# Performance work log

Hardware: AMD Instinct MI355X
Metric: run time of the kernel (lower is better)

The kernel has to match this reference:

```python
import jax, jax.numpy as jnp
import numpy as np

HIDDEN = 128
CHUNK = 3
EPS = 1e-5  # BatchNorm1d eps


def conv1d(x, w, b, pad):
    # x: (B, C_in, S), w: (C_out, C_in, K)
    y = jax.lax.conv_general_dilated(x, w, window_strides=(1,), padding=[(pad, pad)],
                                     dimension_numbers=('NCH', 'OIH', 'NCH'))
    return y + b[None, :, None]


def setup_inputs() -> dict:
    key = jax.random.key(0)
    ks = jax.random.split(key, 16)
    B, S = 64, 2048
    sc = 0.05
    inp = {}
    inp['x'] = jax.random.normal(ks[0], (B, S), jnp.float32)
    inp['seq_lens'] = jax.random.randint(ks[1], (B,), 0, S).astype(jnp.int64)
    # conv stack params (layer 0 has in_channels=1)
    inp['conv_w0'] = jax.random.normal(ks[2], (HIDDEN, 1, 3), jnp.float32) * sc
    inp['conv_b0'] = jax.random.normal(ks[3], (HIDDEN,), jnp.float32) * sc
    inp['conv_w1'] = jax.random.normal(ks[4], (HIDDEN, HIDDEN, 3), jnp.float32) * sc
    inp['conv_b1'] = jax.random.normal(ks[5], (HIDDEN,), jnp.float32) * sc
    inp['conv_w2'] = jax.random.normal(ks[6], (HIDDEN, HIDDEN, 3), jnp.float32) * sc
    inp['conv_b2'] = jax.random.normal(ks[7], (HIDDEN,), jnp.float32) * sc
    # BatchNorm (eval mode): gamma, beta, running mean/var, stacked over 3 layers
    inp['bn_gamma'] = 1.0 + 0.1 * jax.random.normal(ks[8], (3, HIDDEN), jnp.float32)
    inp['bn_beta'] = 0.1 * jax.random.normal(ks[9], (3, HIDDEN), jnp.float32)
    inp['bn_mean'] = 0.1 * jax.random.normal(ks[10], (3, HIDDEN), jnp.float32)
    inp['bn_var'] = jax.random.uniform(ks[11], (3, HIDDEN), jnp.float32, 0.5, 1.5)
    # pre_fc_conv: Conv1d(H, H, kernel=CHUNK) -> consumes whole chunk
    inp['pre_w'] = jax.random.normal(ks[12], (HIDDEN, HIDDEN, CHUNK), jnp.float32) * sc
    inp['pre_b'] = jax.random.normal(ks[13], (HIDDEN,), jnp.float32) * sc
    # fc: Linear(H, 1)
    inp['fc_w'] = jax.random.normal(ks[14], (1, HIDDEN), jnp.float32) * sc
    inp['fc_b'] = jax.random.normal(ks[15], (1,), jnp.float32) * sc
    return inp


def reference(x, seq_lens, conv_w0, conv_b0, conv_w1, conv_b1, conv_w2, conv_b2,
              bn_gamma, bn_beta, bn_mean, bn_var, pre_w, pre_b, fc_w, fc_b):
    h = x[:, None, :]  # (B, 1, S)
    for i, (w, b) in enumerate([(conv_w0, conv_b0), (conv_w1, conv_b1), (conv_w2, conv_b2)]):
        h = jax.nn.relu(conv1d(h, w, b, pad=1))
        # BatchNorm1d in eval mode; Dropout is identity in eval
        scale = (bn_gamma[i] / jnp.sqrt(bn_var[i] + EPS))[None, :, None]
        h = (h - bn_mean[i][None, :, None]) * scale + bn_beta[i][None, :, None]
    h = jnp.transpose(h, (0, 2, 1))  # (B, S, H)
    B, S, H = h.shape
    K = S // CHUNK  # max non-overlapping chunks per sample
    chunks = h[:, :K * CHUNK, :].reshape(B, K, CHUNK, H)  # (B, K, c, H)
    # pre_fc_conv over a length-c chunk with kernel c -> single output position
    z = jnp.einsum('bkth,oht->bko', chunks, pre_w) + pre_b  # (B, K, H)
    z = jax.nn.relu(z)
    out = jnp.einsum('bkh,oh->bko', z, fc_w) + fc_b  # (B, K, 1)
    out = out[..., 0]
    # validity mask: sample b contributes floor(seq_lens[b]/c) chunks
    n_chunks = seq_lens // CHUNK
    valid = jnp.arange(K)[None, :] < n_chunks[:, None]
    out = jnp.where(valid, out, 0.0)
    return out.reshape(-1)  # (B*K,) padded/masked version of torch's ragged concat
```

## Files before the change

kernel.cpp:

```cpp
#include <hip/hip_runtime.h>

#define BB   64
#define S    2048
#define HH   128
#define KCH  682
#define EPS  1e-5f

#define TT2   96
#define NTB2  22
#define NROWS 114

typedef __attribute__((ext_vector_type(8))) _Float16 f16x8;
typedef __attribute__((ext_vector_type(8))) unsigned short u16x8;
typedef __attribute__((ext_vector_type(4))) unsigned short u16x4;
typedef __attribute__((ext_vector_type(4))) float f32x4;

__device__ __forceinline__ unsigned short f2h(float v) {
    union { _Float16 h; unsigned short u; } c;
    c.h = (_Float16)v;
    return c.u;
}

__global__ void pack_w_frags(const float* __restrict__ w1, const float* __restrict__ w2,
                             const float* __restrict__ pw, unsigned short* __restrict__ wpk) {
    int u = blockIdx.x * 256 + threadIdx.x;
    if (u >= 18432) return;
    int lane = u & 63, mc = (u >> 6) & 7, kb = (u >> 9) % 12, mat = u / 6144;
    const float* src = (mat == 0) ? w1 : (mat == 1) ? w2 : pw;
    int c = mc * 16 + (lane & 15);
    int kbase = kb * 32 + ((lane >> 4) << 3);
    u16x8 hv;
    #pragma unroll
    for (int j = 0; j < 8; ++j) {
        int k = kbase + j, tap = k >> 7, ci = k & 127;
        hv[j] = f2h(src[c * 384 + ci * 3 + tap]);
    }
    *(u16x8*)(wpk + (size_t)((mat * 12 + kb) * 8 + mc) * 512 + lane * 8) = hv;
}

__device__ __forceinline__ int read_seqlen(const int* seq, int b) {
    bool is64 = true;
    for (int i = 1; i < 64; i += 2) { if (seq[i] != 0) { is64 = false; break; } }
    return is64 ? seq[2 * b] : seq[b];
}

__device__ __forceinline__ int haddr(int rr, int chunk) {
    return (rr << 8) | ((chunk ^ (rr & 15)) << 4);
}

template<int NT>
__device__ __forceinline__ void conv_f16(
        f32x4 (&acc)[2][NT], const unsigned short* __restrict__ wpk, int mat,
        const unsigned short* __restrict__ hH, int cg, int nt_base, int nt_lim,
        int rbase, int lane) {
    #pragma unroll
    for (int m = 0; m < 2; ++m)
        #pragma unroll
        for (int j = 0; j < NT; ++j) acc[m][j] = (f32x4){0.f, 0.f, 0.f, 0.f};

    const f16x8* wp = (const f16x8*)wpk;
    for (int kb = 0; kb < 12; ++kb) {
        const int fb = (mat * 12 + kb) * 8 + cg * 2;
        f16x8 a0 = wp[(size_t)(fb + 0) * 64 + lane];
        f16x8 a1 = wp[(size_t)(fb + 1) * 64 + lane];
        const int tap = kb >> 2;
        const int chunk = (kb & 3) * 4 + (lane >> 4);
        const int rr0 = rbase + tap + (lane & 15);
        __builtin_amdgcn_s_setprio(1);
        #pragma unroll
        for (int j = 0; j < NT; ++j) {
            const int nt = nt_base + j;
            if (nt < nt_lim) {
                const int ad = haddr(rr0 + nt * 16, chunk);
                f16x8 bh = *(const f16x8*)((const char*)hH + ad);
                acc[0][j] = __builtin_amdgcn_mfma_f32_16x16x32_f16(a0, bh, acc[0][j], 0, 0, 0);
                acc[1][j] = __builtin_amdgcn_mfma_f32_16x16x32_f16(a1, bh, acc[1][j], 0, 0, 0);
            }
        }
        __builtin_amdgcn_s_setprio(0);
    }
}

template<int NT, int ROW_OFF, int T_OFF>
__device__ __forceinline__ void epi_f16(
        f32x4 (&acc)[2][NT], const float* __restrict__ bias,
        const float* __restrict__ bng, const float* __restrict__ bnb,
        const float* __restrict__ bnm, const float* __restrict__ bnv, int layer,
        unsigned short* __restrict__ hH, int cg, int nt_base, int nt_lim,
        int lane, int t0) {
    #pragma unroll
    for (int m = 0; m < 2; ++m) {
        const int c0 = (cg * 2 + m) * 16 + (lane >> 4) * 4;
        const float4 bv = *(const float4*)&bias[c0];
        const float4 g  = *(const float4*)&bng[layer * 128 + c0];
        const float4 be = *(const float4*)&bnb[layer * 128 + c0];
        const float4 mn = *(const float4*)&bnm[layer * 128 + c0];
        const float4 vr = *(const float4*)&bnv[layer * 128 + c0];
        const float av[4] = { g.x * rsqrtf(vr.x + EPS), g.y * rsqrtf(vr.y + EPS),
                              g.z * rsqrtf(vr.z + EPS), g.w * rsqrtf(vr.w + EPS) };
        const float dv[4] = { be.x - mn.x * av[0], be.y - mn.y * av[1],
                              be.z - mn.z * av[2], be.w - mn.w * av[3] };
        const float bb[4] = { bv.x, bv.y, bv.z, bv.w };
        const int byte = c0 * 2, chunk = byte >> 4, off = byte & 15;
        #pragma unroll
        for (int j = 0; j < NT; ++j) {
            const int nt = nt_base + j;
            if (nt < nt_lim) {
                const int tt = nt * 16 + (lane & 15);
                const int t = t0 + T_OFF + tt;
                const int rr = tt + ROW_OFF;
                const bool ok = (t >= 0) && (t < S);
                u16x4 h4;
                #pragma unroll
                for (int r = 0; r < 4; ++r) {
                    float v = 0.f;
                    if (ok) v = fmaf(fmaxf(acc[m][j][r] + bb[r], 0.f), av[r], dv[r]);
                    h4[r] = f2h(v);
                }
                *(u16x4*)((char*)hH + (haddr(rr, chunk) | off)) = h4;
            }
        }
    }
}

__global__ __launch_bounds__(512, 8)
void fused_mfma(const float* __restrict__ x, const int* __restrict__ seq,
                const float* __restrict__ w0, const float* __restrict__ b0,
                const float* __restrict__ b1, const float* __restrict__ b2,
                const float* __restrict__ bng, const float* __restrict__ bnb,
                const float* __restrict__ bnm, const float* __restrict__ bnv,
                const float* __restrict__ pb, const float* __restrict__ fcw,
                const float* __restrict__ fcb, const unsigned short* __restrict__ wpk,
                float* __restrict__ out) {
    __shared__ __align__(16) unsigned short hH[NROWS * 128];
    __shared__ __align__(16) float xs[116];
    __shared__ float p0[6 * 128];
    __shared__ float zred[4][2][16];
    __shared__ int nch_s;

    const int tid = threadIdx.x;
    const int lane = tid & 63, wv = tid >> 6;
    const int cg = wv & 3, ng = wv >> 2;
    const int b  = blockIdx.x / NTB2;
    const int jt = blockIdx.x - b * NTB2;
    const int t0 = jt * TT2;

    if (tid < 116) {
        const int t = t0 - 4 + tid;
        xs[tid] = (t >= 0 && t < S) ? x[b * S + t] : 0.f;
    }
    if (tid < 128) {
        const int c = tid;
        p0[c]         = w0[c * 3 + 0];
        p0[128 + c]   = w0[c * 3 + 1];
        p0[2*128 + c] = w0[c * 3 + 2];
        p0[3*128 + c] = b0[c];
        const float a0 = bng[c] * rsqrtf(bnv[c] + EPS);
        p0[4*128 + c] = a0;
        p0[5*128 + c] = bnb[c] - bnm[c] * a0;
    }
    if (tid == 0) nch_s = read_seqlen(seq, b) / 3;
    __syncthreads();

    for (int it = 0; it < 4; ++it) {
        const int u = tid + it * 512;
        if (u < NROWS * 16) {
            const int rr = u >> 4, oct = u & 15, ci0 = oct * 8;
            const int t = t0 - 3 + rr;
            const bool ok = (t >= 0) && (t < S);
            const float xm = xs[rr], xc = xs[rr + 1], xp = xs[rr + 2];
            u16x8 hv;
            #pragma unroll
            for (int q = 0; q < 8; ++q) {
                const int c = ci0 + q;
                float v = 0.f;
                if (ok) {
                    float sa = fmaf(xp, p0[2*128 + c],
                               fmaf(xc, p0[128 + c],
                               fmaf(xm, p0[c], p0[3*128 + c])));
                    v = fmaf(fmaxf(sa, 0.f), p0[4*128 + c], p0[5*128 + c]);
                }
                hv[q] = f2h(v);
            }
            *(u16x8*)((char*)hH + haddr(rr, oct)) = hv;
        }
    }
    __syncthreads();

    {
        f32x4 acc1[2][4];
        conv_f16<4>(acc1, wpk, 0, hH, cg, ng * 4, 7, 0, lane);
        __syncthreads();
        epi_f16<4, 1, -2>(acc1, b1, bng, bnb, bnm, bnv, 1, hH, cg, ng * 4, 7, lane, t0);
    }
    __syncthreads();

    {
        f32x4 acc2[2][3];
        conv_f16<3>(acc2, wpk, 1, hH, cg, ng * 3, 6, 2, lane);
        __syncthreads();
        epi_f16<3, 3, 0>(acc2, b2, bng, bnb, bnm, bnv, 2, hH, cg, ng * 3, 6, lane, t0);
    }
    __syncthreads();

    f32x4 pacc[2];
    pacc[0] = (f32x4){0.f, 0.f, 0.f, 0.f};
    pacc[1] = (f32x4){0.f, 0.f, 0.f, 0.f};
    {
        const f16x8* wp = (const f16x8*)wpk;
        const int klocal = ng * 16 + (lane & 15);
        for (int kb = 0; kb < 12; ++kb) {
            const int fb = (2 * 12 + kb) * 8 + cg * 2;
            f16x8 a0 = wp[(size_t)(fb + 0) * 64 + lane];
            f16x8 a1 = wp[(size_t)(fb + 1) * 64 + lane];
            const int tap = kb >> 2;
            const int chunk = (kb & 3) * 4 + (lane >> 4);
            const int rr = 3 + 3 * klocal + tap;
            const int ad = haddr(rr, chunk);
            f16x8 bh = *(const f16x8*)((const char*)hH + ad);
            __builtin_amdgcn_s_setprio(1);
            pacc[0] = __builtin_amdgcn_mfma_f32_16x16x32_f16(a0, bh, pacc[0], 0, 0, 0);
            pacc[1] = __builtin_amdgcn_mfma_f32_16x16x32_f16(a1, bh, pacc[1], 0, 0, 0);
            __builtin_amdgcn_s_setprio(0);
        }
    }

    float s0 = 0.f;
    #pragma unroll
    for (int m = 0; m < 2; ++m) {
        const int o0 = (cg * 2 + m) * 16 + (lane >> 4) * 4;
        const float4 pbv = *(const float4*)&pb[o0];
        const float4 fwv = *(const float4*)&fcw[o0];
        const float pbb[4] = { pbv.x, pbv.y, pbv.z, pbv.w };
        const float fww[4] = { fwv.x, fwv.y, fwv.z, fwv.w };
        #pragma unroll
        for (int r = 0; r < 4; ++r)
            s0 += fmaxf(pacc[m][r] + pbb[r], 0.f) * fww[r];
    }
    s0 += __shfl_xor(s0, 16);
    s0 += __shfl_xor(s0, 32);
    if (lane < 16) zred[cg][ng][lane] = s0;
    __syncthreads();
    if (tid < 32) {
        const int kt = tid >> 4, kl = tid & 15;
        const float zz = zred[0][kt][kl] + zred[1][kt][kl]
                       + zred[2][kt][kl] + zred[3][kt][kl];
        const int kG = jt * 32 + tid;
        if (kG < KCH)
            out[b * KCH + kG] = (kG < nch_s) ? (zz + fcb[0]) : 0.f;
    }
}

#define TT   78
#define NTB  27
#define STRIDE 84

__device__ __forceinline__ void stage_w_fb(float* __restrict__ wtS,
                                           const float* __restrict__ wraw, int cc, int tid) {
    for (int i = tid; i < 6144; i += 256)
        wtS[i] = wraw[(i & 127) * 384 + cc * 3 + (i >> 7)];
}

__device__ __forceinline__ void conv_gemm_fb(float (&acc)[10][4],
                                             const float* __restrict__ wraw,
                                             const float* __restrict__ hAp,
                                             float* __restrict__ wtS,
                                             int tid, int c0, int tbase) {
    #pragma unroll
    for (int i = 0; i < 10; ++i)
        #pragma unroll
        for (int q = 0; q < 4; ++q) acc[i][q] = 0.f;
    for (int cc = 0; cc < HH; cc += 16) {
        __syncthreads();
        stage_w_fb(wtS, wraw, cc, tid);
        __syncthreads();
        for (int ci = 0; ci < 16; ++ci) {
            float hr[12];
            #pragma unroll
            for (int j = 0; j < 12; ++j) hr[j] = hAp[(cc + ci) * STRIDE + tbase + j];
            #pragma unroll
            for (int tap = 0; tap < 3; ++tap) {
                const float4 w = *(const float4*)&wtS[((ci * 3 + tap) << 7) + c0];
                #pragma unroll
                for (int i = 0; i < 10; ++i) {
                    const float h = hr[i + tap];
                    acc[i][0] = fmaf(h, w.x, acc[i][0]);
                    acc[i][1] = fmaf(h, w.y, acc[i][1]);
                    acc[i][2] = fmaf(h, w.z, acc[i][2]);
                    acc[i][3] = fmaf(h, w.w, acc[i][3]);
                }
            }
        }
    }
}

__global__ __launch_bounds__(256, 2)
void fused_pd(const float* __restrict__ x, const int* __restrict__ seq,
              const float* __restrict__ w0, const float* __restrict__ b0,
              const float* __restrict__ w1raw, const float* __restrict__ b1,
              const float* __restrict__ w2raw, const float* __restrict__ b2,
              const float* __restrict__ bng, const float* __restrict__ bnb,
              const float* __restrict__ bnm, const float* __restrict__ bnv,
              const float* __restrict__ pwraw, const float* __restrict__ pb,
              const float* __restrict__ fcw, const float* __restrict__ fcb,
              float* __restrict__ out) {
    __shared__ __align__(16) float hA[HH * STRIDE];
    __shared__ __align__(16) float wtS[6144];
    __shared__ __align__(16) float xsf[TT + 8];
    __shared__ int nch_s;

    const int tid = threadIdx.x;
    const int b  = blockIdx.x / NTB;
    const int jt = blockIdx.x - b * NTB;
    const int t0 = jt * TT;

    for (int j = tid; j < TT + 6; j += 256) {
        const int t = t0 - 3 + j;
        xsf[j] = (t >= 0 && t < S) ? x[b * S + t] : 0.f;
    }
    if (tid == 0) nch_s = read_seqlen(seq, b) / 3;

    const int cch = tid & 127;
    const float w0a = w0[cch * 3 + 0], w0b = w0[cch * 3 + 1], w0c = w0[cch * 3 + 2];
    const float bb0 = b0[cch];
    const float a0 = bng[cch] * rsqrtf(bnv[cch] + EPS);
    const float d0 = bnb[cch] - bnm[cch] * a0;
    __syncthreads();

    for (int i = tid; i < (TT + 4) * HH; i += 256) {
        const int ttl = i >> 7;
        const int t = t0 - 2 + ttl;
        float v = 0.f;
        if (t >= 0 && t < S) {
            float sa = fmaf(xsf[ttl + 2], w0c, fmaf(xsf[ttl + 1], w0b, fmaf(xsf[ttl], w0a, bb0)));
            v = fmaf(fmaxf(sa, 0.f), a0, d0);
        }
        hA[cch * STRIDE + ttl] = v;
    }

    const int cg = tid & 31, tg = tid >> 5;
    const int c0 = cg * 4;
    const int tbase = tg * 10;
    float acc[10][4];

    conv_gemm_fb(acc, w1raw, hA, wtS, tid, c0, tbase);
    {
        const float4 bv = *(const float4*)&b1[c0];
        const float4 g  = *(const float4*)&bng[HH + c0];
        const float4 be = *(const float4*)&bnb[HH + c0];
        const float4 mn = *(const float4*)&bnm[HH + c0];
        const float4 vr = *(const float4*)&bnv[HH + c0];
        float av[4] = { g.x * rsqrtf(vr.x + EPS), g.y * rsqrtf(vr.y + EPS),
                        g.z * rsqrtf(vr.z + EPS), g.w * rsqrtf(vr.w + EPS) };
        float dv[4] = { be.x - mn.x * av[0], be.y - mn.y * av[1],
                        be.z - mn.z * av[2], be.w - mn.w * av[3] };
        float bb[4] = { bv.x, bv.y, bv.z, bv.w };
        __syncthreads();
        #pragma unroll
        for (int i = 0; i < 10; ++i) {
            const int tt2 = tbase + i;
            const int t = t0 - 1 + tt2;
            const bool ok = (t >= 0) && (t < S);
            #pragma unroll
            for (int q = 0; q < 4; ++q) {
                float v = 0.f;
                if (ok) v = fmaf(fmaxf(acc[i][q] + bb[q], 0.f), av[q], dv[q]);
                hA[(c0 + q) * STRIDE + tt2] = v;
            }
        }
        __syncthreads();
    }

    conv_gemm_fb(acc, w2raw, hA, wtS, tid, c0, tbase);
    {
        const float4 bv = *(const float4*)&b2[c0];
        const float4 g  = *(const float4*)&bng[2 * HH + c0];
        const float4 be = *(const float4*)&bnb[2 * HH + c0];
        const float4 mn = *(const float4*)&bnm[2 * HH + c0];
        const float4 vr = *(const float4*)&bnv[2 * HH + c0];
        float av[4] = { g.x * rsqrtf(vr.x + EPS), g.y * rsqrtf(vr.y + EPS),
                        g.z * rsqrtf(vr.z + EPS), g.w * rsqrtf(vr.w + EPS) };
        float dv[4] = { be.x - mn.x * av[0], be.y - mn.y * av[1],
                        be.z - mn.z * av[2], be.w - mn.w * av[3] };
        float bb[4] = { bv.x, bv.y, bv.z, bv.w };
        __syncthreads();
        #pragma unroll
        for (int i = 0; i < 10; ++i) {
            const int tt3 = tbase + i;
            if (tt3 < TT) {
                const int t = t0 + tt3;
                #pragma unroll
                for (int q = 0; q < 4; ++q) {
                    float vv = 0.f;
                    if (t < S) vv = fmaf(fmaxf(acc[i][q] + bb[q], 0.f), av[q], dv[q]);
                    hA[(c0 + q) * STRIDE + tt3] = vv;
                }
            }
        }
        __syncthreads();
    }

    const int og = tid & 31, kg = tid >> 5;
    const int oo = og * 4;
    float pacc[4][4];
    #pragma unroll
    for (int j = 0; j < 4; ++j)
        #pragma unroll
        for (int q = 0; q < 4; ++q) pacc[j][q] = 0.f;

    for (int hc = 0; hc < HH; hc += 16) {
        __syncthreads();
        stage_w_fb(wtS, pwraw, hc, tid);
        __syncthreads();
        for (int h = 0; h < 16; ++h) {
            #pragma unroll
            for (int tap = 0; tap < 3; ++tap) {
                const float4 w = *(const float4*)&wtS[((h * 3 + tap) << 7) + oo];
                #pragma unroll
                for (int j = 0; j < 4; ++j) {
                    int kl = kg * 4 + j; kl = (kl > 25) ? 25 : kl;
                    const float hv = hA[(hc + h) * STRIDE + 3 * kl + tap];
                    pacc[j][0] = fmaf(hv, w.x, pacc[j][0]);
                    pacc[j][1] = fmaf(hv, w.y, pacc[j][1]);
                    pacc[j][2] = fmaf(hv, w.z, pacc[j][2]);
                    pacc[j][3] = fmaf(hv, w.w, pacc[j][3]);
                }
            }
        }
    }

    const float fcb0 = fcb[0];
    const float4 pbv = *(const float4*)&pb[oo];
    const float4 fwv = *(const float4*)&fcw[oo];
    const int nch = nch_s;
    #pragma unroll
    for (int j = 0; j < 4; ++j) {
        float s = fmaxf(pacc[j][0] + pbv.x, 0.f) * fwv.x
                + fmaxf(pacc[j][1] + pbv.y, 0.f) * fwv.y
                + fmaxf(pacc[j][2] + pbv.z, 0.f) * fwv.z
                + fmaxf(pacc[j][3] + pbv.w, 0.f) * fwv.w;
        #pragma unroll
        for (int m = 1; m < 32; m <<= 1) s += __shfl_xor(s, m, 64);
        if (og == 0) {
            const int kl = kg * 4 + j;
            const int kG = jt * 26 + kl;
            if (kl < 26 && kG < KCH)
                out[b * KCH + kG] = (kG < nch) ? (s + fcb0) : 0.f;
        }
    }
}

extern "C" void kernel_launch(void* const* d_in, const int* in_sizes, int n_in,
                              void* d_out, int out_size, void* d_ws, size_t ws_size,
                              hipStream_t stream) {
    (void)in_sizes; (void)n_in; (void)out_size;
    const float* x    = (const float*)d_in[0];
    const int*   seq  = (const int*)d_in[1];
    const float* w0   = (const float*)d_in[2];
    const float* b0   = (const float*)d_in[3];
    const float* w1   = (const float*)d_in[4];
    const float* b1   = (const float*)d_in[5];
    const float* w2   = (const float*)d_in[6];
    const float* b2   = (const float*)d_in[7];
    const float* bng  = (const float*)d_in[8];
    const float* bnb  = (const float*)d_in[9];
    const float* bnm  = (const float*)d_in[10];
    const float* bnv  = (const float*)d_in[11];
    const float* pw   = (const float*)d_in[12];
    const float* pb   = (const float*)d_in[13];
    const float* fcw  = (const float*)d_in[14];
    const float* fcb  = (const float*)d_in[15];
    float* out = (float*)d_out;

    const size_t need = (size_t)3 * 12 * 8 * 1024;
    if (ws_size >= need) {
        unsigned short* wpk = (unsigned short*)d_ws;
        pack_w_frags<<<72, 256, 0, stream>>>(w1, w2, pw, wpk);
        fused_mfma<<<BB * NTB2, 512, 0, stream>>>(x, seq, w0, b0, b1, b2,
                                                  bng, bnb, bnm, bnv,
                                                  pb, fcw, fcb, wpk, out);
    } else {
        fused_pd<<<BB * NTB, 256, 0, stream>>>(x, seq, w0, b0, w1, b1, w2, b2,
                                               bng, bnb, bnm, bnv, pw, pb, fcw, fcb,
                                               out);
    }
}
```

Baseline: 77.58 us.

## Stage weight fragments through double-buffered LDS instead of per-wave global loads

Weight MFMA fragments were previously read from global memory by each wave, so waves sharing a channel group loaded the same fragments repeatedly. Now each k-block slice is loaded once per block cooperatively into a double-buffered LDS stage, prefetching the next slice while computing the current one. This cuts redundant global/L2 traffic but adds 16KB of LDS per block, a __syncthreads per k-step, and lowers the launch-bounds occupancy hint from 8 to 6.

```diff
diff --git a/kernel.cpp b/kernel.cpp
--- a/kernel.cpp
+++ b/kernel.cpp
@@ -49,20 +49,29 @@
 }
 
 template<int NT>
-__device__ __forceinline__ void conv_f16(
+__device__ __forceinline__ void conv_st(
         f32x4 (&acc)[2][NT], const unsigned short* __restrict__ wpk, int mat,
-        const unsigned short* __restrict__ hH, int cg, int nt_base, int nt_lim,
-        int rbase, int lane) {
+        const unsigned short* __restrict__ hH, unsigned short* __restrict__ aStage,
+        int cg, int wv, int nt_base, int nt_lim, int rbase, int lane) {
     #pragma unroll
     for (int m = 0; m < 2; ++m)
         #pragma unroll
         for (int j = 0; j < NT; ++j) acc[m][j] = (f32x4){0.f, 0.f, 0.f, 0.f};
 
-    const f16x8* wp = (const f16x8*)wpk;
+    const char* gb = (const char*)wpk + (size_t)(mat * 12) * 8192;
+    {
+        uint4 t = *(const uint4*)(gb + (size_t)wv * 1024 + lane * 16);
+        *(uint4*)((char*)aStage + wv * 1024 + lane * 16) = t;
+    }
+    __syncthreads();
     for (int kb = 0; kb < 12; ++kb) {
-        const int fb = (mat * 12 + kb) * 8 + cg * 2;
-        f16x8 a0 = wp[(size_t)(fb + 0) * 64 + lane];
-        f16x8 a1 = wp[(size_t)(fb + 1) * 64 + lane];
+        const int buf = kb & 1;
+        const bool more = (kb < 11);
+        uint4 tnext;
+        if (more)
+            tnext = *(const uint4*)(gb + (size_t)(kb + 1) * 8192 + (size_t)wv * 1024 + lane * 16);
+        f16x8 a0 = *(const f16x8*)((const char*)aStage + buf * 8192 + (cg * 2 + 0) * 1024 + lane * 16);
+        f16x8 a1 = *(const f16x8*)((const char*)aStage + buf * 8192 + (cg * 2 + 1) * 1024 + lane * 16);
         const int tap = kb >> 2;
         const int chunk = (kb & 3) * 4 + (lane >> 4);
         const int rr0 = rbase + tap + (lane & 15);
@@ -78,6 +87,9 @@
             }
         }
         __builtin_amdgcn_s_setprio(0);
+        if (more)
+            *(uint4*)((char*)aStage + (buf ^ 1) * 8192 + wv * 1024 + lane * 16) = tnext;
+        __syncthreads();
     }
 }
 
@@ -123,7 +135,7 @@
     }
 }
 
-__global__ __launch_bounds__(512, 8)
+__global__ __launch_bounds__(512, 6)
 void fused_mfma(const float* __restrict__ x, const int* __restrict__ seq,
                 const float* __restrict__ w0, const float* __restrict__ b0,
                 const float* __restrict__ b1, const float* __restrict__ b2,
@@ -133,6 +145,7 @@
                 const float* __restrict__ fcb, const unsigned short* __restrict__ wpk,
                 float* __restrict__ out) {
     __shared__ __align__(16) unsigned short hH[NROWS * 128];
+    __shared__ __align__(16) unsigned short aStage[2][4096];
     __shared__ __align__(16) float xs[116];
     __shared__ float p0[6 * 128];
     __shared__ float zred[4][2][16];
@@ -189,16 +202,14 @@
 
     {
         f32x4 acc1[2][4];
-        conv_f16<4>(acc1, wpk, 0, hH, cg, ng * 4, 7, 0, lane);
-        __syncthreads();
+        conv_st<4>(acc1, wpk, 0, hH, &aStage[0][0], cg, wv, ng * 4, 7, 0, lane);
         epi_f16<4, 1, -2>(acc1, b1, bng, bnb, bnm, bnv, 1, hH, cg, ng * 4, 7, lane, t0);
     }
     __syncthreads();
 
     {
         f32x4 acc2[2][3];
-        conv_f16<3>(acc2, wpk, 1, hH, cg, ng * 3, 6, 2, lane);
-        __syncthreads();
+        conv_st<3>(acc2, wpk, 1, hH, &aStage[0][0], cg, wv, ng * 3, 6, 2, lane);
         epi_f16<3, 3, 0>(acc2, b2, bng, bnb, bnm, bnv, 2, hH, cg, ng * 3, 6, lane, t0);
     }
     __syncthreads();
@@ -207,12 +218,21 @@
     pacc[0] = (f32x4){0.f, 0.f, 0.f, 0.f};
     pacc[1] = (f32x4){0.f, 0.f, 0.f, 0.f};
     {
-        const f16x8* wp = (const f16x8*)wpk;
+        const char* gb = (const char*)wpk + (size_t)(2 * 12) * 8192;
         const int klocal = ng * 16 + (lane & 15);
+        {
+            uint4 t = *(const uint4*)(gb + (size_t)wv * 1024 + lane * 16);
+            *(uint4*)((char*)aStage + wv * 1024 + lane * 16) = t;
+        }
+        __syncthreads();
         for (int kb = 0; kb < 12; ++kb) {
-            const int fb = (2 * 12 + kb) * 8 + cg * 2;
-            f16x8 a0 = wp[(size_t)(fb + 0) * 64 + lane];
-            f16x8 a1 = wp[(size_t)(fb + 1) * 64 + lane];
+            const int buf = kb & 1;
+            const bool more = (kb < 11);
+            uint4 tnext;
+            if (more)
+                tnext = *(const uint4*)(gb + (size_t)(kb + 1) * 8192 + (size_t)wv * 1024 + lane * 16);
+            f16x8 a0 = *(const f16x8*)((const char*)aStage + buf * 8192 + (cg * 2 + 0) * 1024 + lane * 16);
+            f16x8 a1 = *(const f16x8*)((const char*)aStage + buf * 8192 + (cg * 2 + 1) * 1024 + lane * 16);
             const int tap = kb >> 2;
             const int chunk = (kb & 3) * 4 + (lane >> 4);
             const int rr = 3 + 3 * klocal + tap;
@@ -222,6 +242,9 @@
             pacc[0] = __builtin_amdgcn_mfma_f32_16x16x32_f16(a0, bh, pacc[0], 0, 0, 0);
             pacc[1] = __builtin_amdgcn_mfma_f32_16x16x32_f16(a1, bh, pacc[1], 0, 0, 0);
             __builtin_amdgcn_s_setprio(0);
+            if (more)
+                *(uint4*)((char*)aStage + (buf ^ 1) * 8192 + wv * 1024 + lane * 16) = tnext;
+            __syncthreads();
         }
     }
 
```

New measurement: 79.21 us. 1.02x slower.
